# Kernel tuning notes

Measured on AMD Instinct MI355X. Metric: run time of the kernel, lower is better.

Reference implementation:

```python
import jax, jax.numpy as jnp
import numpy as np

B, T, N, H = 256, 128, 512, 512
LB, UB = 0.0, 0.1
MAX_IT = 32  # bounded substitute for the data-dependent while loop (converges in a few iters)


def setup_inputs() -> dict:
    key = jax.random.key(0)
    ks = jax.random.split(key, 11)
    s = 1.0 / np.sqrt(H)
    u = lambda k, shape: jax.random.uniform(k, shape, jnp.float32, -s, s)
    return {
        "x": jax.random.normal(ks[0], (B, T, N), jnp.float32),
        "W_ih0": u(ks[1], (3 * H, N)), "W_hh0": u(ks[2], (3 * H, H)),
        "b_ih0": u(ks[3], (3 * H,)), "b_hh0": u(ks[4], (3 * H,)),
        "W_ih1": u(ks[5], (3 * H, H)), "W_hh1": u(ks[6], (3 * H, H)),
        "b_ih1": u(ks[7], (3 * H,)), "b_hh1": u(ks[8], (3 * H,)),
        "fc_w": u(ks[9], (N, H)), "fc_b": u(ks[10], (N,)),
    }


def gru_layer(x, W_ih, W_hh, b_ih, b_hh):
    # x: [B, T, I] -> hidden sequence [B, T, H]; matches torch.nn.GRU gate math.
    xi = jnp.einsum('bti,gi->btg', x, W_ih) + b_ih  # precompute input proj [B,T,3H]

    def step(h, xi_t):
        gh = h @ W_hh.T + b_hh
        xr, xz, xn = jnp.split(xi_t, 3, axis=-1)
        hr, hz, hn = jnp.split(gh, 3, axis=-1)
        r = jax.nn.sigmoid(xr + hr)
        z = jax.nn.sigmoid(xz + hz)
        n = jnp.tanh(xn + r * hn)
        h2 = (1.0 - z) * n + z * h
        return h2, h2

    h0 = jnp.zeros((x.shape[0], H), x.dtype)
    _, hs = jax.lax.scan(step, h0, jnp.swapaxes(xi, 0, 1))
    return jnp.swapaxes(hs, 0, 1)


def rebalance(w):
    # Water-filling: clamp to [LB, UB], redistribute clipped mass to non-capped
    # names proportionally, repeat until no weight exceeds UB. Bounded iteration
    # count with masked no-op updates (do-while semantics: body runs at least once).
    wc0 = jnp.clip(w, LB, UB)

    def body(st, _):
        old, wc, cont = st
        leftover = jnp.sum(old - wc)
        mask = wc != UB
        noms = jnp.where(mask, wc, 0.0)
        gift = leftover * noms / jnp.sum(noms)
        wc2 = wc + gift                      # gift is 0 where mask is False
        again = jnp.any(wc2 > UB)
        wc_next = jnp.where(again, jnp.clip(wc2, LB, UB), wc2)
        old_n = jnp.where(cont, wc2, old)
        wc_n = jnp.where(cont, wc_next, wc)
        return (old_n, wc_n, jnp.logical_and(cont, again)), None

    (old, wc, _), _ = jax.lax.scan(body, (w, wc0, jnp.array(True)), None, length=MAX_IT)
    return wc


def reference(x, W_ih0, W_hh0, b_ih0, b_hh0, W_ih1, W_hh1, b_ih1, b_hh1, fc_w, fc_b):
    h = gru_layer(x, W_ih0, W_hh0, b_ih0, b_hh0)
    h = gru_layer(h, W_ih1, W_hh1, b_ih1, b_hh1)
    h_t = h[:, -1, :]                        # last timestep [B, H]
    logit = h_t @ fc_w.T + fc_b              # dropout is identity in eval
    logit = jax.nn.softmax(jax.nn.silu(logit), axis=-1)
    return jax.vmap(rebalance)(logit)
```

## Files before the change

### kernel.cpp

```cpp
#include <hip/hip_runtime.h>
#include <math.h>

#define BB 256
#define TT 128
#define NN 512
#define HH 512
#define G3 1536
#define SLAB (HH * BB)
#define XSLAB (G3 * BB)
#define CH 16

typedef __attribute__((ext_vector_type(8))) short bf16x8;
typedef __attribute__((ext_vector_type(4))) float f32x4;
typedef unsigned short ushort;

__device__ __forceinline__ ushort bf16_rne(float f) {
    union { float f; unsigned u; } v; v.f = f;
    unsigned r = (v.u + 0x7fffu + ((v.u >> 16) & 1u)) >> 16;
    return (ushort)r;
}
__device__ __forceinline__ float bf16_tof(ushort h) {
    union { float f; unsigned u; } v; v.u = ((unsigned)h) << 16;
    return v.f;
}
__device__ __forceinline__ float sigm(float v) { return 1.f / (1.f + expf(-v)); }

__global__ void zero_kernel(float* p, int n) {
    int i = blockIdx.x * blockDim.x + threadIdx.x;
    if (i < n) p[i] = 0.f;
}

__global__ __launch_bounds__(256) void convert_split(
    const float* __restrict__ in, ushort* __restrict__ hi,
    ushort* __restrict__ lo, int n) {
    int i = (blockIdx.x * 256 + threadIdx.x) * 4;
    if (i >= n) return;
    float4 v = *(const float4*)(in + i);
    float f[4] = {v.x, v.y, v.z, v.w};
    ushort h[4], l[4];
#pragma unroll
    for (int q = 0; q < 4; ++q) {
        ushort hh = bf16_rne(f[q]);
        h[q] = hh;
        l[q] = bf16_rne(f[q] - bf16_tof(hh));
    }
    *(ushort4*)(hi + i) = *(ushort4*)h;
    *(ushort4*)(lo + i) = *(ushort4*)l;
}

__global__ __launch_bounds__(64) void pack_swz(
    const float* __restrict__ Whh0, const float* __restrict__ Wih1,
    const float* __restrict__ Whh1, ushort* __restrict__ pk) {
    const int bi = blockIdx.x;
    const int it = bi & 3, kq = (bi >> 2) & 3, p = (bi >> 4) & 31, sec = bi >> 9;
    const float* W = (sec == 0) ? Whh0 : (sec == 1) ? Wih1 : Whh1;
    const int lane = threadIdx.x;
    const int l15 = lane & 15, l4 = lane >> 4;
    ushort* base = pk + (size_t)bi * 3072 + lane * 8;
#pragma unroll
    for (int g = 0; g < 3; ++g) {
        int grow = g * 512 + p * 16 + l15;
        const float* src = W + (size_t)grow * 512 + kq * 128 + it * 32 + l4 * 8;
        ushort hs[8], ls[8];
#pragma unroll
        for (int e = 0; e < 8; ++e) {
            float v = src[e];
            ushort h = bf16_rne(v);
            hs[e] = h;
            ls[e] = bf16_rne(v - bf16_tof(h));
        }
        *(uint4*)(base + g * 1024) = *(uint4*)hs;
        *(uint4*)(base + g * 1024 + 512) = *(uint4*)ls;
    }
}

__global__ __launch_bounds__(256) void xi_mfma_x(
    const ushort* __restrict__ Wh, const ushort* __restrict__ Wl,
    const float* __restrict__ x, int t0,
    const float* __restrict__ bias, float* __restrict__ out) {
    __shared__ ushort As[2][128][40];
    __shared__ ushort Bs[2][128][40];
    const int tid = threadIdx.x;
    const int n0 = blockIdx.x * 128;
    const int g0 = blockIdx.y * 128;
    const int tl = n0 >> 8, b0 = n0 & 255;
    const int tg = t0 + tl;
    const int w = tid >> 6, lane = tid & 63;
    const int wg = (w >> 1) * 64, wb = (w & 1) * 64;
    const int l15 = lane & 15, l4 = lane >> 4;
    const int sr = tid >> 2, sc = (tid & 3) * 8;

    f32x4 acc[4][4] = {};
    for (int kc = 0; kc < 512; kc += 32) {
        uint4 a0 = *(const uint4*)(Wh + (size_t)(g0 + sr) * 512 + kc + sc);
        uint4 a1 = *(const uint4*)(Wh + (size_t)(g0 + 64 + sr) * 512 + kc + sc);
        uint4 a2 = *(const uint4*)(Wl + (size_t)(g0 + sr) * 512 + kc + sc);
        uint4 a3 = *(const uint4*)(Wl + (size_t)(g0 + 64 + sr) * 512 + kc + sc);
        const float* xr0 = x + ((size_t)(b0 + sr) * TT + tg) * NN + kc + sc;
        const float* xr1 = x + ((size_t)(b0 + 64 + sr) * TT + tg) * NN + kc + sc;
        float4 f00 = *(const float4*)xr0, f01 = *(const float4*)(xr0 + 4);
        float4 f10 = *(const float4*)xr1, f11 = *(const float4*)(xr1 + 4);
        float fa[8] = {f00.x, f00.y, f00.z, f00.w, f01.x, f01.y, f01.z, f01.w};
        float fb[8] = {f10.x, f10.y, f10.z, f10.w, f11.x, f11.y, f11.z, f11.w};
        ushort h0v[8], l0v[8], h1v[8], l1v[8];
#pragma unroll
        for (int q = 0; q < 8; ++q) {
            ushort hh = bf16_rne(fa[q]);
            h0v[q] = hh; l0v[q] = bf16_rne(fa[q] - bf16_tof(hh));
            hh = bf16_rne(fb[q]);
            h1v[q] = hh; l1v[q] = bf16_rne(fb[q] - bf16_tof(hh));
        }
        __syncthreads();
        *(uint4*)&As[0][sr][sc] = a0;      *(uint4*)&As[0][64 + sr][sc] = a1;
        *(uint4*)&As[1][sr][sc] = a2;      *(uint4*)&As[1][64 + sr][sc] = a3;
        *(uint4*)&Bs[0][sr][sc] = *(uint4*)h0v;  *(uint4*)&Bs[0][64 + sr][sc] = *(uint4*)h1v;
        *(uint4*)&Bs[1][sr][sc] = *(uint4*)l0v;  *(uint4*)&Bs[1][64 + sr][sc] = *(uint4*)l1v;
        __syncthreads();
        bf16x8 ah[4], al[4], bh[4], bl[4];
#pragma unroll
        for (int i = 0; i < 4; ++i) {
            ah[i] = *(const bf16x8*)&As[0][wg + 16 * i + l15][l4 * 8];
            al[i] = *(const bf16x8*)&As[1][wg + 16 * i + l15][l4 * 8];
            bh[i] = *(const bf16x8*)&Bs[0][wb + 16 * i + l15][l4 * 8];
            bl[i] = *(const bf16x8*)&Bs[1][wb + 16 * i + l15][l4 * 8];
        }
#pragma unroll
        for (int i = 0; i < 4; ++i)
#pragma unroll
            for (int j = 0; j < 4; ++j) {
                acc[i][j] = __builtin_amdgcn_mfma_f32_16x16x32_bf16(ah[i], bh[j], acc[i][j], 0, 0, 0);
                acc[i][j] = __builtin_amdgcn_mfma_f32_16x16x32_bf16(ah[i], bl[j], acc[i][j], 0, 0, 0);
                acc[i][j] = __builtin_amdgcn_mfma_f32_16x16x32_bf16(al[i], bh[j], acc[i][j], 0, 0, 0);
            }
    }
    float* op = out + (size_t)tl * XSLAB;
#pragma unroll
    for (int i = 0; i < 4; ++i) {
        int gbase = g0 + wg + 16 * i + l4 * 4;
#pragma unroll
        for (int r = 0; r < 4; ++r) {
            float bv = bias[gbase + r];
#pragma unroll
            for (int j = 0; j < 4; ++j)
                op[(size_t)(gbase + r) * 256 + b0 + wb + 16 * j + l15] = acc[i][j][r] + bv;
        }
    }
}

__device__ __forceinline__ void kreduce(float* scr, int kq, int ct, int l15, int l4,
                                        f32x4 acc[3]) {
    const int slot = (kq >> 1) * 2 + ct;
    const int pos0 = (l4 * 4) * 17 + l15;
    __syncthreads();
    if (kq & 1) {
#pragma unroll
        for (int g = 0; g < 3; ++g)
#pragma unroll
            for (int q = 0; q < 4; ++q)
                scr[slot * 816 + g * 272 + pos0 + q * 17] = acc[g][q];
    }
    __syncthreads();
    if (!(kq & 1)) {
#pragma unroll
        for (int g = 0; g < 3; ++g)
#pragma unroll
            for (int q = 0; q < 4; ++q)
                acc[g][q] += scr[slot * 816 + g * 272 + pos0 + q * 17];
    }
    if (kq == 2) {
#pragma unroll
        for (int g = 0; g < 3; ++g)
#pragma unroll
            for (int q = 0; q < 4; ++q)
                scr[(2 + ct) * 816 + g * 272 + pos0 + q * 17] = acc[g][q];
    }
    __syncthreads();
    if (kq == 0) {
#pragma unroll
        for (int g = 0; g < 3; ++g)
#pragma unroll
            for (int q = 0; q < 4; ++q)
                acc[g][q] += scr[(2 + ct) * 816 + g * 272 + pos0 + q * 17];
    }
}

__device__ __forceinline__ void epi_xi(float* __restrict__ xo,
    const float* __restrict__ bias, int p, int b0, int kq, int ct, int l15, int l4,
    const f32x4 acc[3]) {
    if (kq != 0) return;
    const int b = b0 + ct * 16 + l15;
#pragma unroll
    for (int g = 0; g < 3; ++g)
#pragma unroll
        for (int q = 0; q < 4; ++q) {
            int grow = g * 512 + p * 16 + l4 * 4 + q;
            xo[(size_t)grow * 256 + b] = acc[g][q] + bias[grow];
        }
}

__device__ __forceinline__ void epi_gru(const float* __restrict__ xi,
    const float* __restrict__ bhh, const float* __restrict__ hpv,
    float* __restrict__ hnew, ushort* __restrict__ Hh, ushort* __restrict__ Hl,
    int p, int b0, int kq, int ct, int l15, int l4, const f32x4 acc[3]) {
    if (kq != 0) return;
    const int b = b0 + ct * 16 + l15;
    ushort hq[4], lq[4];
#pragma unroll
    for (int q = 0; q < 4; ++q) {
        int jrow = p * 16 + l4 * 4 + q;
        float xr = xi[(size_t)jrow * 256 + b];
        float xz = xi[(size_t)(512 + jrow) * 256 + b];
        float xn = xi[(size_t)(1024 + jrow) * 256 + b];
        float hp = hpv[(size_t)jrow * 256 + b];
        float rr = sigm(xr + acc[0][q] + bhh[jrow]);
        float zz = sigm(xz + acc[1][q] + bhh[512 + jrow]);
        float nn = tanhf(xn + rr * (acc[2][q] + bhh[1024 + jrow]));
        float hv = (1.f - zz) * nn + zz * hp;
        hnew[(size_t)jrow * 256 + b] = hv;
        ushort hh = bf16_rne(hv);
        hq[q] = hh;
        lq[q] = bf16_rne(hv - bf16_tof(hh));
    }
    size_t o = (size_t)b * 512 + p * 16 + l4 * 4;
    *(ushort4*)(Hh + o) = *(ushort4*)hq;
    *(ushort4*)(Hl + o) = *(ushort4*)lq;
}

__global__ __launch_bounds__(512) void step_v10(
    int s, const ushort* __restrict__ pk,
    const float* __restrict__ xi0, float* __restrict__ xi1,
    const float* __restrict__ bih1,
    const float* __restrict__ bhh0, const float* __restrict__ bhh1,
    float* __restrict__ h0f, float* __restrict__ h1f,
    ushort* __restrict__ H0h, ushort* __restrict__ H0l,
    ushort* __restrict__ H1h, ushort* __restrict__ H1l) {
    __shared__ float scr[3264];
    const int bi = blockIdx.x;
    const int sec = bi >> 8, local = bi & 255;
    const int t = (sec == 0) ? s : (sec == 1) ? s - 1 : s - 2;
    if (t < 0 || t > 127) return;
    const int p = (local & 7) * 4 + ((local >> 3) & 3);
    const int b0 = (local >> 5) * 32;
    const int tid = threadIdx.x, w = tid >> 6, lane = tid & 63;
    const int l15 = lane & 15, l4 = lane >> 4;
    const int kq = w >> 1, ct = w & 1;

    const ushort *Bh, *Bl;
    if (sec == 0)      { int sl = (t - 1) & 1; Bh = H0h + (size_t)sl * SLAB; Bl = H0l + (size_t)sl * SLAB; }
    else if (sec == 1) { int sl = t & 1;       Bh = H0h + (size_t)sl * SLAB; Bl = H0l + (size_t)sl * SLAB; }
    else               { int sl = (t - 1) & 1; Bh = H1h + (size_t)sl * SLAB; Bl = H1l + (size_t)sl * SLAB; }

    const ushort* baseA = pk + (size_t)((sec * 32 + p) * 4 + kq) * 12288 + lane * 8;
    const int brow = b0 + ct * 16 + l15;
    const ushort* bhp = Bh + (size_t)brow * 512 + kq * 128 + l4 * 8;
    const ushort* blp = Bl + (size_t)brow * 512 + kq * 128 + l4 * 8;

    f32x4 acc[3] = {};
#pragma unroll
    for (int it = 0; it < 4; ++it) {
        bf16x8 bh = *(const bf16x8*)(bhp + it * 32);
        bf16x8 bl = *(const bf16x8*)(blp + it * 32);
#pragma unroll
        for (int g = 0; g < 3; ++g) {
            const ushort* rec = baseA + (it * 3 + g) * 1024;
            bf16x8 ah = *(const bf16x8*)rec;
            bf16x8 al = *(const bf16x8*)(rec + 512);
            acc[g] = __builtin_amdgcn_mfma_f32_16x16x32_bf16(ah, bh, acc[g], 0, 0, 0);
            acc[g] = __builtin_amdgcn_mfma_f32_16x16x32_bf16(ah, bl, acc[g], 0, 0, 0);
            acc[g] = __builtin_amdgcn_mfma_f32_16x16x32_bf16(al, bh, acc[g], 0, 0, 0);
        }
    }
    kreduce(scr, kq, ct, l15, l4, acc);
    if (sec == 1) {
        epi_xi(xi1 + (size_t)(t & 1) * XSLAB, bih1, p, b0, kq, ct, l15, l4, acc);
    } else if (sec == 0) {
        epi_gru(xi0 + (size_t)(t & (CH - 1)) * XSLAB, bhh0,
                h0f + (size_t)((t - 1) & 1) * SLAB, h0f + (size_t)(t & 1) * SLAB,
                H0h + (size_t)(t & 1) * SLAB, H0l + (size_t)(t & 1) * SLAB,
                p, b0, kq, ct, l15, l4, acc);
    } else {
        epi_gru(xi1 + (size_t)(t & 1) * XSLAB, bhh1,
                h1f + (size_t)((t - 1) & 1) * SLAB, h1f + (size_t)(t & 1) * SLAB,
                H1h + (size_t)(t & 1) * SLAB, H1l + (size_t)(t & 1) * SLAB,
                p, b0, kq, ct, l15, l4, acc);
    }
}


__global__ __launch_bounds__(256) void hT_to_h(
    const float* __restrict__ hT, float* __restrict__ h) {
    __shared__ float tb[64][65];
    const int tid = threadIdx.x;
    const int k0 = blockIdx.x * 64, b0 = blockIdx.y * 64;
#pragma unroll
    for (int i = 0; i < 4; ++i) {
        int r = (tid >> 4) + 16 * i, c = (tid & 15) * 4;
        float4 v = *(const float4*)(hT + (size_t)(k0 + r) * 256 + b0 + c);
        tb[c + 0][r] = v.x; tb[c + 1][r] = v.y; tb[c + 2][r] = v.z; tb[c + 3][r] = v.w;
    }
    __syncthreads();
#pragma unroll
    for (int i = 0; i < 4; ++i) {
        int r = (tid >> 4) + 16 * i, c = (tid & 15) * 4;
        float4 v;
        v.x = tb[r][c]; v.y = tb[r][c + 1]; v.z = tb[r][c + 2]; v.w = tb[r][c + 3];
        *(float4*)(h + (size_t)(b0 + r) * 512 + k0 + c) = v;
    }
}

__device__ __forceinline__ float blockReduceSum(float v, float* tmp) {
    __syncthreads();
#pragma unroll
    for (int o = 32; o; o >>= 1) v += __shfl_down(v, o);
    if ((threadIdx.x & 63) == 0) tmp[threadIdx.x >> 6] = v;
    __syncthreads();
    if (threadIdx.x == 0) tmp[4] = tmp[0] + tmp[1] + tmp[2] + tmp[3];
    __syncthreads();
    return tmp[4];
}

__device__ __forceinline__ float blockReduceMax(float v, float* tmp) {
    __syncthreads();
#pragma unroll
    for (int o = 32; o; o >>= 1) v = fmaxf(v, __shfl_down(v, o));
    if ((threadIdx.x & 63) == 0) tmp[threadIdx.x >> 6] = v;
    __syncthreads();
    if (threadIdx.x == 0) tmp[4] = fmaxf(fmaxf(tmp[0], tmp[1]), fmaxf(tmp[2], tmp[3]));
    __syncthreads();
    return tmp[4];
}

__global__ __launch_bounds__(256) void head_kernel(
    const float* __restrict__ h1, const float* __restrict__ fcw,
    const float* __restrict__ fcb, float* __restrict__ out) {
    __shared__ __align__(16) float hrow[512];
    __shared__ float wv[512];
    __shared__ float ov[512];
    __shared__ float tmp[8];
    const int b = blockIdx.x, tid = threadIdx.x;
    hrow[tid]       = h1[(size_t)b * 512 + tid];
    hrow[tid + 256] = h1[(size_t)b * 512 + 256 + tid];
    __syncthreads();

    float s[2];
#pragma unroll
    for (int q = 0; q < 2; ++q) {
        int n = tid + q * 256;
        const float* wr = fcw + (size_t)n * 512;
        float acc = 0.f;
        for (int k = 0; k < 512; k += 4) {
            float4 wq = *(const float4*)(wr + k);
            acc += wq.x * hrow[k] + wq.y * hrow[k + 1] + wq.z * hrow[k + 2] + wq.w * hrow[k + 3];
        }
        float l = acc + fcb[n];
        s[q] = l / (1.f + expf(-l));
    }

    float mx = blockReduceMax(fmaxf(s[0], s[1]), tmp);
    float e0 = expf(s[0] - mx), e1 = expf(s[1] - mx);
    float sum = blockReduceSum(e0 + e1, tmp);
    float w0 = e0 / sum, w1 = e1 / sum;

    ov[tid] = w0;       ov[tid + 256] = w1;
    wv[tid]       = fminf(fmaxf(w0, 0.f), 0.1f);
    wv[tid + 256] = fminf(fmaxf(w1, 0.f), 0.1f);
    __syncthreads();

    for (int it = 0; it < 32; ++it) {
        float wc0 = wv[tid], wc1 = wv[tid + 256];
        float o0 = ov[tid], o1 = ov[tid + 256];
        float leftover = blockReduceSum((o0 - wc0) + (o1 - wc1), tmp);
        float n0 = (wc0 != 0.1f) ? wc0 : 0.f;
        float n1 = (wc1 != 0.1f) ? wc1 : 0.f;
        float denom = blockReduceSum(n0 + n1, tmp);
        float w20 = wc0 + leftover * n0 / denom;
        float w21 = wc1 + leftover * n1 / denom;
        float fl = ((w20 > 0.1f) || (w21 > 0.1f)) ? 1.f : 0.f;
        bool again = blockReduceSum(fl, tmp) > 0.f;
        __syncthreads();
        ov[tid] = w20; ov[tid + 256] = w21;
        wv[tid]       = again ? fminf(fmaxf(w20, 0.f), 0.1f) : w20;
        wv[tid + 256] = again ? fminf(fmaxf(w21, 0.f), 0.1f) : w21;
        __syncthreads();
        if (!again) break;
    }

    out[(size_t)b * 512 + tid]       = wv[tid];
    out[(size_t)b * 512 + 256 + tid] = wv[tid + 256];
}

extern "C" void kernel_launch(void* const* d_in, const int* in_sizes, int n_in,
                              void* d_out, int out_size, void* d_ws, size_t ws_size,
                              hipStream_t stream) {
    const float* x    = (const float*)d_in[0];
    const float* Wih0 = (const float*)d_in[1];
    const float* Whh0 = (const float*)d_in[2];
    const float* bih0 = (const float*)d_in[3];
    const float* bhh0 = (const float*)d_in[4];
    const float* Wih1 = (const float*)d_in[5];
    const float* Whh1 = (const float*)d_in[6];
    const float* bih1 = (const float*)d_in[7];
    const float* bhh1 = (const float*)d_in[8];
    const float* fcw  = (const float*)d_in[9];
    const float* fcb  = (const float*)d_in[10];
    float* out = (float*)d_out;

    const size_t WHALF = (size_t)G3 * HH;
    ushort* W0h = (ushort*)d_ws;
    ushort* W0l = W0h + WHALF;
    ushort* pk  = W0l + WHALF;
    float* xi0 = (float*)(pk + (size_t)1536 * 3072);
    float* xi1 = xi0 + (size_t)CH * XSLAB;
    float* h0f = xi1 + 2 * (size_t)XSLAB;
    float* h1f = h0f + 2 * (size_t)SLAB;
    float* h1n = h1f + 2 * (size_t)SLAB;
    ushort* H0h = (ushort*)(h1n + SLAB);
    ushort* H0l = H0h + 2 * (size_t)SLAB;
    ushort* H1h = H0l + 2 * (size_t)SLAB;
    ushort* H1l = H1h + 2 * (size_t)SLAB;

    convert_split<<<(G3 * HH) / 1024, 256, 0, stream>>>(Wih0, W0h, W0l, G3 * HH);
    pack_swz<<<1536, 64, 0, stream>>>(Whh0, Wih1, Whh1, pk);
    zero_kernel<<<SLAB / 256, 256, 0, stream>>>(h0f + SLAB, SLAB);
    zero_kernel<<<SLAB / 256, 256, 0, stream>>>(h1f + SLAB, SLAB);
    zero_kernel<<<(SLAB / 2) / 256, 256, 0, stream>>>((float*)(H0h + SLAB), SLAB / 2);
    zero_kernel<<<(SLAB / 2) / 256, 256, 0, stream>>>((float*)(H0l + SLAB), SLAB / 2);
    zero_kernel<<<(SLAB / 2) / 256, 256, 0, stream>>>((float*)(H1h + SLAB), SLAB / 2);
    zero_kernel<<<(SLAB / 2) / 256, 256, 0, stream>>>((float*)(H1l + SLAB), SLAB / 2);

    for (int c = 0; c < TT / CH; ++c) {
        xi_mfma_x<<<dim3(CH * 2, 12), 256, 0, stream>>>(W0h, W0l, x, c * CH, bih0, xi0);
        for (int tl = 0; tl < CH; ++tl) {
            int s = c * CH + tl;
            step_v10<<<768, 512, 0, stream>>>(s, pk, xi0, xi1, bih1, bhh0, bhh1,
                                              h0f, h1f, H0h, H0l, H1h, H1l);
        }
    }
    step_v10<<<768, 512, 0, stream>>>(128, pk, xi0, xi1, bih1, bhh0, bhh1,
                                      h0f, h1f, H0h, H0l, H1h, H1l);
    step_v10<<<768, 512, 0, stream>>>(129, pk, xi0, xi1, bih1, bhh0, bhh1,
                                      h0f, h1f, H0h, H0l, H1h, H1l);

    hT_to_h<<<dim3(8, 4), 256, 0, stream>>>(h1f + SLAB, h1n);
    head_kernel<<<BB, 256, 0, stream>>>(h1n, fcw, fcb, out);
}
```

Baseline: 2.165 ms.

## Fuse layer-1 input projection into layer-1 recurrent step, shortening pipeline by one stage

```diff
diff --git a/kernel.cpp b/kernel.cpp
--- a/kernel.cpp
+++ b/kernel.cpp
@@ -25,9 +25,16 @@
 }
 __device__ __forceinline__ float sigm(float v) { return 1.f / (1.f + expf(-v)); }
 
-__global__ void zero_kernel(float* p, int n) {
-    int i = blockIdx.x * blockDim.x + threadIdx.x;
-    if (i < n) p[i] = 0.f;
+__global__ __launch_bounds__(256) void zero6(
+    float* h0s, float* h1s, ushort* H0hs, ushort* H0ls, ushort* H1hs, ushort* H1ls) {
+    int i = blockIdx.x * 256 + threadIdx.x;
+    int sel = i / 65536, r = i % 65536;
+    if (sel == 0)      ((float2*)h0s)[r] = {0.f, 0.f};
+    else if (sel == 1) ((float2*)h1s)[r] = {0.f, 0.f};
+    else if (sel == 2) { if (r < 32768) ((uint2*)H0hs)[r] = {0u, 0u}; }
+    else if (sel == 3) { if (r < 32768) ((uint2*)H0ls)[r] = {0u, 0u}; }
+    else if (sel == 4) { if (r < 32768) ((uint2*)H1hs)[r] = {0u, 0u}; }
+    else               { if (r < 32768) ((uint2*)H1ls)[r] = {0u, 0u}; }
 }
 
 __global__ __launch_bounds__(256) void convert_split(
@@ -147,142 +154,179 @@
     }
 }
 
-__device__ __forceinline__ void kreduce(float* scr, int kq, int ct, int l15, int l4,
-                                        f32x4 acc[3]) {
+template <int NG>
+__device__ __forceinline__ void kreduceN(float* scr, int kq, int ct, int l15, int l4,
+                                         f32x4* acc) {
+    const int SS = NG * 272;
     const int slot = (kq >> 1) * 2 + ct;
     const int pos0 = (l4 * 4) * 17 + l15;
     __syncthreads();
     if (kq & 1) {
 #pragma unroll
-        for (int g = 0; g < 3; ++g)
+        for (int g = 0; g < NG; ++g)
 #pragma unroll
             for (int q = 0; q < 4; ++q)
-                scr[slot * 816 + g * 272 + pos0 + q * 17] = acc[g][q];
+                scr[slot * SS + g * 272 + pos0 + q * 17] = acc[g][q];
     }
     __syncthreads();
     if (!(kq & 1)) {
 #pragma unroll
-        for (int g = 0; g < 3; ++g)
+        for (int g = 0; g < NG; ++g)
 #pragma unroll
             for (int q = 0; q < 4; ++q)
-                acc[g][q] += scr[slot * 816 + g * 272 + pos0 + q * 17];
+                acc[g][q] += scr[slot * SS + g * 272 + pos0 + q * 17];
     }
     if (kq == 2) {
 #pragma unroll
-        for (int g = 0; g < 3; ++g)
+        for (int g = 0; g < NG; ++g)
 #pragma unroll
             for (int q = 0; q < 4; ++q)
-                scr[(2 + ct) * 816 + g * 272 + pos0 + q * 17] = acc[g][q];
+                scr[(2 + ct) * SS + g * 272 + pos0 + q * 17] = acc[g][q];
     }
     __syncthreads();
     if (kq == 0) {
 #pragma unroll
-        for (int g = 0; g < 3; ++g)
+        for (int g = 0; g < NG; ++g)
 #pragma unroll
             for (int q = 0; q < 4; ++q)
-                acc[g][q] += scr[(2 + ct) * 816 + g * 272 + pos0 + q * 17];
-    }
-}
-
-__device__ __forceinline__ void epi_xi(float* __restrict__ xo,
-    const float* __restrict__ bias, int p, int b0, int kq, int ct, int l15, int l4,
-    const f32x4 acc[3]) {
-    if (kq != 0) return;
-    const int b = b0 + ct * 16 + l15;
-#pragma unroll
-    for (int g = 0; g < 3; ++g)
-#pragma unroll
-        for (int q = 0; q < 4; ++q) {
-            int grow = g * 512 + p * 16 + l4 * 4 + q;
-            xo[(size_t)grow * 256 + b] = acc[g][q] + bias[grow];
-        }
-}
-
-__device__ __forceinline__ void epi_gru(const float* __restrict__ xi,
-    const float* __restrict__ bhh, const float* __restrict__ hpv,
-    float* __restrict__ hnew, ushort* __restrict__ Hh, ushort* __restrict__ Hl,
-    int p, int b0, int kq, int ct, int l15, int l4, const f32x4 acc[3]) {
-    if (kq != 0) return;
-    const int b = b0 + ct * 16 + l15;
-    ushort hq[4], lq[4];
-#pragma unroll
-    for (int q = 0; q < 4; ++q) {
-        int jrow = p * 16 + l4 * 4 + q;
-        float xr = xi[(size_t)jrow * 256 + b];
-        float xz = xi[(size_t)(512 + jrow) * 256 + b];
-        float xn = xi[(size_t)(1024 + jrow) * 256 + b];
-        float hp = hpv[(size_t)jrow * 256 + b];
-        float rr = sigm(xr + acc[0][q] + bhh[jrow]);
-        float zz = sigm(xz + acc[1][q] + bhh[512 + jrow]);
-        float nn = tanhf(xn + rr * (acc[2][q] + bhh[1024 + jrow]));
-        float hv = (1.f - zz) * nn + zz * hp;
-        hnew[(size_t)jrow * 256 + b] = hv;
-        ushort hh = bf16_rne(hv);
-        hq[q] = hh;
-        lq[q] = bf16_rne(hv - bf16_tof(hh));
-    }
-    size_t o = (size_t)b * 512 + p * 16 + l4 * 4;
-    *(ushort4*)(Hh + o) = *(ushort4*)hq;
-    *(ushort4*)(Hl + o) = *(ushort4*)lq;
-}
-
-__global__ __launch_bounds__(512) void step_v10(
+                acc[g][q] += scr[(2 + ct) * SS + g * 272 + pos0 + q * 17];
+    }
+}
+
+__global__ __launch_bounds__(512) void step_v11(
     int s, const ushort* __restrict__ pk,
-    const float* __restrict__ xi0, float* __restrict__ xi1,
+    const float* __restrict__ xi0,
     const float* __restrict__ bih1,
     const float* __restrict__ bhh0, const float* __restrict__ bhh1,
     float* __restrict__ h0f, float* __restrict__ h1f,
     ushort* __restrict__ H0h, ushort* __restrict__ H0l,
     ushort* __restrict__ H1h, ushort* __restrict__ H1l) {
-    __shared__ float scr[3264];
+    __shared__ float scr[6528];
     const int bi = blockIdx.x;
     const int sec = bi >> 8, local = bi & 255;
-    const int t = (sec == 0) ? s : (sec == 1) ? s - 1 : s - 2;
+    const int t = (sec == 0) ? s : s - 1;
     if (t < 0 || t > 127) return;
     const int p = (local & 7) * 4 + ((local >> 3) & 3);
     const int b0 = (local >> 5) * 32;
     const int tid = threadIdx.x, w = tid >> 6, lane = tid & 63;
     const int l15 = lane & 15, l4 = lane >> 4;
     const int kq = w >> 1, ct = w & 1;
-
-    const ushort *Bh, *Bl;
-    if (sec == 0)      { int sl = (t - 1) & 1; Bh = H0h + (size_t)sl * SLAB; Bl = H0l + (size_t)sl * SLAB; }
-    else if (sec == 1) { int sl = t & 1;       Bh = H0h + (size_t)sl * SLAB; Bl = H0l + (size_t)sl * SLAB; }
-    else               { int sl = (t - 1) & 1; Bh = H1h + (size_t)sl * SLAB; Bl = H1l + (size_t)sl * SLAB; }
-
-    const ushort* baseA = pk + (size_t)((sec * 32 + p) * 4 + kq) * 12288 + lane * 8;
     const int brow = b0 + ct * 16 + l15;
-    const ushort* bhp = Bh + (size_t)brow * 512 + kq * 128 + l4 * 8;
-    const ushort* blp = Bl + (size_t)brow * 512 + kq * 128 + l4 * 8;
-
-    f32x4 acc[3] = {};
-#pragma unroll
-    for (int it = 0; it < 4; ++it) {
-        bf16x8 bh = *(const bf16x8*)(bhp + it * 32);
-        bf16x8 bl = *(const bf16x8*)(blp + it * 32);
-#pragma unroll
-        for (int g = 0; g < 3; ++g) {
-            const ushort* rec = baseA + (it * 3 + g) * 1024;
-            bf16x8 ah = *(const bf16x8*)rec;
-            bf16x8 al = *(const bf16x8*)(rec + 512);
-            acc[g] = __builtin_amdgcn_mfma_f32_16x16x32_bf16(ah, bh, acc[g], 0, 0, 0);
-            acc[g] = __builtin_amdgcn_mfma_f32_16x16x32_bf16(ah, bl, acc[g], 0, 0, 0);
-            acc[g] = __builtin_amdgcn_mfma_f32_16x16x32_bf16(al, bh, acc[g], 0, 0, 0);
-        }
-    }
-    kreduce(scr, kq, ct, l15, l4, acc);
-    if (sec == 1) {
-        epi_xi(xi1 + (size_t)(t & 1) * XSLAB, bih1, p, b0, kq, ct, l15, l4, acc);
-    } else if (sec == 0) {
-        epi_gru(xi0 + (size_t)(t & (CH - 1)) * XSLAB, bhh0,
-                h0f + (size_t)((t - 1) & 1) * SLAB, h0f + (size_t)(t & 1) * SLAB,
-                H0h + (size_t)(t & 1) * SLAB, H0l + (size_t)(t & 1) * SLAB,
-                p, b0, kq, ct, l15, l4, acc);
+
+    if (sec == 0) {
+        const int sl = (t - 1) & 1;
+        const ushort* Bh = H0h + (size_t)sl * SLAB;
+        const ushort* Bl = H0l + (size_t)sl * SLAB;
+        const ushort* baseA = pk + (size_t)((0 * 32 + p) * 4 + kq) * 12288 + lane * 8;
+        const ushort* bhp = Bh + (size_t)brow * 512 + kq * 128 + l4 * 8;
+        const ushort* blp = Bl + (size_t)brow * 512 + kq * 128 + l4 * 8;
+        f32x4 acc[3] = {};
+#pragma unroll
+        for (int it = 0; it < 4; ++it) {
+            bf16x8 bh = *(const bf16x8*)(bhp + it * 32);
+            bf16x8 bl = *(const bf16x8*)(blp + it * 32);
+#pragma unroll
+            for (int g = 0; g < 3; ++g) {
+                const ushort* rec = baseA + (it * 3 + g) * 1024;
+                bf16x8 ah = *(const bf16x8*)rec;
+                bf16x8 al = *(const bf16x8*)(rec + 512);
+                acc[g] = __builtin_amdgcn_mfma_f32_16x16x32_bf16(ah, bh, acc[g], 0, 0, 0);
+                acc[g] = __builtin_amdgcn_mfma_f32_16x16x32_bf16(ah, bl, acc[g], 0, 0, 0);
+                acc[g] = __builtin_amdgcn_mfma_f32_16x16x32_bf16(al, bh, acc[g], 0, 0, 0);
+            }
+        }
+        kreduceN<3>(scr, kq, ct, l15, l4, acc);
+        if (kq == 0) {
+            const float* xi = xi0 + (size_t)(t & (CH - 1)) * XSLAB;
+            const float* hpv = h0f + (size_t)((t - 1) & 1) * SLAB;
+            float* hnew = h0f + (size_t)(t & 1) * SLAB;
+            ushort* Hh = H0h + (size_t)(t & 1) * SLAB;
+            ushort* Hl = H0l + (size_t)(t & 1) * SLAB;
+            const int b = brow;
+            ushort hq[4], lq[4];
+#pragma unroll
+            for (int q = 0; q < 4; ++q) {
+                int jrow = p * 16 + l4 * 4 + q;
+                float xr = xi[(size_t)jrow * 256 + b];
+                float xz = xi[(size_t)(512 + jrow) * 256 + b];
+                float xn = xi[(size_t)(1024 + jrow) * 256 + b];
+                float hp = hpv[(size_t)jrow * 256 + b];
+                float rr = sigm(xr + acc[0][q] + bhh0[jrow]);
+                float zz = sigm(xz + acc[1][q] + bhh0[512 + jrow]);
+                float nn = tanhf(xn + rr * (acc[2][q] + bhh0[1024 + jrow]));
+                float hv = (1.f - zz) * nn + zz * hp;
+                hnew[(size_t)jrow * 256 + b] = hv;
+                ushort hh = bf16_rne(hv);
+                hq[q] = hh;
+                lq[q] = bf16_rne(hv - bf16_tof(hh));
+            }
+            size_t o = (size_t)b * 512 + p * 16 + l4 * 4;
+            *(ushort4*)(Hh + o) = *(ushort4*)hq;
+            *(ushort4*)(Hl + o) = *(ushort4*)lq;
+        }
     } else {
-        epi_gru(xi1 + (size_t)(t & 1) * XSLAB, bhh1,
-                h1f + (size_t)((t - 1) & 1) * SLAB, h1f + (size_t)(t & 1) * SLAB,
-                H1h + (size_t)(t & 1) * SLAB, H1l + (size_t)(t & 1) * SLAB,
-                p, b0, kq, ct, l15, l4, acc);
+        const int slX = t & 1, slG = (t - 1) & 1;
+        const ushort* BhX = H0h + (size_t)slX * SLAB;
+        const ushort* BlX = H0l + (size_t)slX * SLAB;
+        const ushort* BhG = H1h + (size_t)slG * SLAB;
+        const ushort* BlG = H1l + (size_t)slG * SLAB;
+        const ushort* baseAX = pk + (size_t)((1 * 32 + p) * 4 + kq) * 12288 + lane * 8;
+        const ushort* baseAG = pk + (size_t)((2 * 32 + p) * 4 + kq) * 12288 + lane * 8;
+        const ushort* bhpX = BhX + (size_t)brow * 512 + kq * 128 + l4 * 8;
+        const ushort* blpX = BlX + (size_t)brow * 512 + kq * 128 + l4 * 8;
+        const ushort* bhpG = BhG + (size_t)brow * 512 + kq * 128 + l4 * 8;
+        const ushort* blpG = BlG + (size_t)brow * 512 + kq * 128 + l4 * 8;
+        f32x4 acc[6] = {};
+#pragma unroll
+        for (int it = 0; it < 4; ++it) {
+            bf16x8 bhX = *(const bf16x8*)(bhpX + it * 32);
+            bf16x8 blX = *(const bf16x8*)(blpX + it * 32);
+            bf16x8 bhG = *(const bf16x8*)(bhpG + it * 32);
+            bf16x8 blG = *(const bf16x8*)(blpG + it * 32);
+#pragma unroll
+            for (int g = 0; g < 3; ++g) {
+                const ushort* recX = baseAX + (it * 3 + g) * 1024;
+                const ushort* recG = baseAG + (it * 3 + g) * 1024;
+                bf16x8 ahX = *(const bf16x8*)recX;
+                bf16x8 alX = *(const bf16x8*)(recX + 512);
+                bf16x8 ahG = *(const bf16x8*)recG;
+                bf16x8 alG = *(const bf16x8*)(recG + 512);
+                acc[g] = __builtin_amdgcn_mfma_f32_16x16x32_bf16(ahX, bhX, acc[g], 0, 0, 0);
+                acc[g] = __builtin_amdgcn_mfma_f32_16x16x32_bf16(ahX, blX, acc[g], 0, 0, 0);
+                acc[g] = __builtin_amdgcn_mfma_f32_16x16x32_bf16(alX, bhX, acc[g], 0, 0, 0);
+                acc[3 + g] = __builtin_amdgcn_mfma_f32_16x16x32_bf16(ahG, bhG, acc[3 + g], 0, 0, 0);
+                acc[3 + g] = __builtin_amdgcn_mfma_f32_16x16x32_bf16(ahG, blG, acc[3 + g], 0, 0, 0);
+                acc[3 + g] = __builtin_amdgcn_mfma_f32_16x16x32_bf16(alG, bhG, acc[3 + g], 0, 0, 0);
+            }
+        }
+        kreduceN<6>(scr, kq, ct, l15, l4, acc);
+        if (kq == 0) {
+            const float* hpv = h1f + (size_t)((t - 1) & 1) * SLAB;
+            float* hnew = h1f + (size_t)(t & 1) * SLAB;
+            ushort* Hh = H1h + (size_t)(t & 1) * SLAB;
+            ushort* Hl = H1l + (size_t)(t & 1) * SLAB;
+            const int b = brow;
+            ushort hq[4], lq[4];
+#pragma unroll
+            for (int q = 0; q < 4; ++q) {
+                int jrow = p * 16 + l4 * 4 + q;
+                float xr = acc[0][q] + bih1[jrow];
+                float xz = acc[1][q] + bih1[512 + jrow];
+                float xn = acc[2][q] + bih1[1024 + jrow];
+                float hp = hpv[(size_t)jrow * 256 + b];
+                float rr = sigm(xr + acc[3][q] + bhh1[jrow]);
+                float zz = sigm(xz + acc[4][q] + bhh1[512 + jrow]);
+                float nn = tanhf(xn + rr * (acc[5][q] + bhh1[1024 + jrow]));
+                float hv = (1.f - zz) * nn + zz * hp;
+                hnew[(size_t)jrow * 256 + b] = hv;
+                ushort hh = bf16_rne(hv);
+                hq[q] = hh;
+                lq[q] = bf16_rne(hv - bf16_tof(hh));
+            }
+            size_t o = (size_t)b * 512 + p * 16 + l4 * 4;
+            *(ushort4*)(Hh + o) = *(ushort4*)hq;
+            *(ushort4*)(Hl + o) = *(ushort4*)lq;
+        }
     }
 }
 
@@ -410,8 +454,7 @@
     ushort* W0l = W0h + WHALF;
     ushort* pk  = W0l + WHALF;
     float* xi0 = (float*)(pk + (size_t)1536 * 3072);
-    float* xi1 = xi0 + (size_t)CH * XSLAB;
-    float* h0f = xi1 + 2 * (size_t)XSLAB;
+    float* h0f = xi0 + (size_t)CH * XSLAB;
     float* h1f = h0f + 2 * (size_t)SLAB;
     float* h1n = h1f + 2 * (size_t)SLAB;
     ushort* H0h = (ushort*)(h1n + SLAB);
@@ -421,24 +464,18 @@
 
     convert_split<<<(G3 * HH) / 1024, 256, 0, stream>>>(Wih0, W0h, W0l, G3 * HH);
     pack_swz<<<1536, 64, 0, stream>>>(Whh0, Wih1, Whh1, pk);
-    zero_kernel<<<SLAB / 256, 256, 0, stream>>>(h0f + SLAB, SLAB);
-    zero_kernel<<<SLAB / 256, 256, 0, stream>>>(h1f + SLAB, SLAB);
-    zero_kernel<<<(SLAB / 2) / 256, 256, 0, stream>>>((float*)(H0h + SLAB), SLAB / 2);
-    zero_kernel<<<(SLAB / 2) / 256, 256, 0, stream>>>((float*)(H0l + SLAB), SLAB / 2);
-    zero_kernel<<<(SLAB / 2) / 256, 256, 0, stream>>>((float*)(H1h + SLAB), SLAB / 2);
-    zero_kernel<<<(SLAB / 2) / 256, 256, 0, stream>>>((float*)(H1l + SLAB), SLAB / 2);
+    zero6<<<1536, 256, 0, stream>>>(h0f + SLAB, h1f + SLAB,
+                                    H0h + SLAB, H0l + SLAB, H1h + SLAB, H1l + SLAB);
 
     for (int c = 0; c < TT / CH; ++c) {
         xi_mfma_x<<<dim3(CH * 2, 12), 256, 0, stream>>>(W0h, W0l, x, c * CH, bih0, xi0);
         for (int tl = 0; tl < CH; ++tl) {
             int s = c * CH + tl;
-            step_v10<<<768, 512, 0, stream>>>(s, pk, xi0, xi1, bih1, bhh0, bhh1,
+            step_v11<<<512, 512, 0, stream>>>(s, pk, xi0, bih1, bhh0, bhh1,
                                               h0f, h1f, H0h, H0l, H1h, H1l);
         }
     }
-    step_v10<<<768, 512, 0, stream>>>(128, pk, xi0, xi1, bih1, bhh0, bhh1,
-                                      h0f, h1f, H0h, H0l, H1h, H1l);
-    step_v10<<<768, 512, 0, stream>>>(129, pk, xi0, xi1, bih1, bhh0, bhh1,
+    step_v11<<<512, 512, 0, stream>>>(128, pk, xi0, bih1, bhh0, bhh1,
                                       h0f, h1f, H0h, H0l, H1h, H1l);
 
     hT_to_h<<<dim3(8, 4), 256, 0, stream>>>(h1f + SLAB, h1n);
```

Measured after the change: 2.196 ms. Within noise of the previous version (+1.4%).
